# Optimization experiments

Measured on AMD Instinct MI355X. Metric: run time of the kernel, lower is better.

Reference implementation:

```python
import jax, jax.numpy as jnp
import numpy as np

S, R, CM, CZ, C, H = 128, 256, 256, 128, 32, 8
EPS = 1e-5


def layer_norm(x, w, b):
    mu = jnp.mean(x, axis=-1, keepdims=True)
    var = jnp.mean(jnp.square(x - mu), axis=-1, keepdims=True)
    return (x - mu) * jax.lax.rsqrt(var + EPS) * w + b


def setup_inputs() -> dict:
    key = jax.random.key(0)
    ks = jax.random.split(key, 10)
    s = 0.02
    return {
        "m": jax.random.normal(ks[0], (S, R, CM), jnp.float32),
        "z": jax.random.normal(ks[1], (R, R, CZ), jnp.float32),
        "ln_m_w": jnp.ones((CM,), jnp.float32),
        "ln_m_b": jnp.zeros((CM,), jnp.float32),
        "ln_z_w": jnp.ones((CZ,), jnp.float32),
        "ln_z_b": jnp.zeros((CZ,), jnp.float32),
        "Wz": jax.random.normal(ks[2], (CZ, H), jnp.float32) * s,
        "Wq": jax.random.normal(ks[3], (CM, H * C), jnp.float32) * s,
        "Wk": jax.random.normal(ks[4], (CM, H * C), jnp.float32) * s,
        "Wv": jax.random.normal(ks[5], (CM, H * C), jnp.float32) * s,
        "Wg": jax.random.normal(ks[6], (CM, H * C), jnp.float32) * s,
        "bg": jnp.ones((H * C,), jnp.float32),
        "Wo": jax.random.normal(ks[7], (H * C, CM), jnp.float32) * s,
        "bo": jnp.zeros((CM,), jnp.float32),
    }


def reference(m, z, ln_m_w, ln_m_b, ln_z_w, ln_z_b, Wz, Wq, Wk, Wv, Wg, bg, Wo, bo):
    mn = layer_norm(m, ln_m_w, ln_m_b)              # [S,R,CM]
    zn = layer_norm(z, ln_z_w, ln_z_b)              # [R,R,CZ]
    bias = jnp.einsum('qkz,zh->hqk', zn, Wz)        # [H,R,R] pair bias
    q = (mn @ Wq).reshape(S, R, H, C) * (C ** -0.5)
    k = (mn @ Wk).reshape(S, R, H, C)
    v = (mn @ Wv).reshape(S, R, H, C)
    logits = jnp.einsum('sqhc,skhc->shqk', q, k) + bias[None]  # [S,H,R,R]
    a = jax.nn.softmax(logits, axis=-1)
    o = jnp.einsum('shqk,skhc->sqhc', a, v)         # [S,R,H,C]
    g = jax.nn.sigmoid(mn @ Wg + bg).reshape(S, R, H, C)
    return (g * o).reshape(S, R, H * C) @ Wo + bo   # [S,R,CM]
```

## Files before the change

kernel.cpp:

```cpp
#include <hip/hip_runtime.h>
#include <math.h>

#define S_DIM 128
#define R_DIM 256
#define CM_DIM 256
#define CZ_DIM 128
#define C_DIM 32
#define H_DIM 8
#define HC_DIM 256
#define LN_EPS 1e-5f
#define ZPAD 132
#define HSZ 1048576
#define BIAS_SCALE 16384.0f
#define BIAS_INV (1.0f / 16384.0f)

typedef _Float16 half8 __attribute__((ext_vector_type(8)));
typedef _Float16 half4 __attribute__((ext_vector_type(4)));
typedef float f32x4 __attribute__((ext_vector_type(4)));
typedef short short4v __attribute__((ext_vector_type(4)));
typedef short short8v __attribute__((ext_vector_type(8)));

__device__ __forceinline__ float wave_sum(float v) {
#pragma unroll
    for (int off = 32; off > 0; off >>= 1) v += __shfl_down(v, off);
    return v;
}

__device__ __forceinline__ void gload16(const _Float16* src, _Float16* dst) {
    __builtin_amdgcn_global_load_lds((const __attribute__((address_space(1))) void*)src,
                                     (__attribute__((address_space(3))) void*)dst, 16, 0, 0);
}

__global__ __launch_bounds__(256) void convert_w_kernel(const float* __restrict__ Wq,
                                                        const float* __restrict__ Wk,
                                                        const float* __restrict__ Wv,
                                                        const float* __restrict__ Wg,
                                                        const float* __restrict__ Wo,
                                                        _Float16* __restrict__ w3) {
    int kb = blockIdx.x;
    int mat = blockIdx.y;
    const float* src = (mat == 0) ? Wq : (mat == 1) ? Wk : (mat == 2) ? Wv : (mat == 3) ? Wg : Wo;
    int n = threadIdx.x;
    _Float16 tmp[32];
#pragma unroll
    for (int kk = 0; kk < 32; kk++)
        tmp[kk] = (_Float16)src[(size_t)(kb * 32 + kk) * 256 + n];
    half8* dst = (half8*)(w3 + (size_t)mat * 65536 + (size_t)kb * 8192 + (size_t)n * 32);
#pragma unroll
    for (int i = 0; i < 4; i++) dst[i] = *(half8*)&tmp[i * 8];
}

__global__ __launch_bounds__(64) void prep_wz_kernel(const float* __restrict__ w,
                                                     const float* __restrict__ b,
                                                     const float* __restrict__ Wz,
                                                     float* __restrict__ u_g,
                                                     float* __restrict__ UB) {
    int lane = threadIdx.x;
    float w0 = w[lane], w1 = w[lane + 64];
    float b0 = b[lane], b1 = b[lane + 64];
#pragma unroll
    for (int h = 0; h < H_DIM; h++) {
        float wz0 = Wz[lane * H_DIM + h], wz1 = Wz[(lane + 64) * H_DIM + h];
        float u0 = w0 * wz0, u1 = w1 * wz1;
        u_g[h * ZPAD + lane] = u0;
        u_g[h * ZPAD + lane + 64] = u1;
        float U = wave_sum(u0 + u1);
        float B = wave_sum(b0 * wz0 + b1 * wz1);
        if (lane == 0) { UB[h] = U; UB[8 + h] = B; }
    }
}

__global__ __launch_bounds__(64) void ln_m_kernel(const float* __restrict__ m,
                                                  const float* __restrict__ w,
                                                  const float* __restrict__ b,
                                                  _Float16* __restrict__ mn) {
    int row = blockIdx.x;
    int t = threadIdx.x;
    const float4* mrow = (const float4*)(m + (size_t)row * CM_DIM);
    float4 x = mrow[t];
    float s = x.x + x.y + x.z + x.w;
    float ss = x.x * x.x + x.y * x.y + x.z * x.z + x.w * x.w;
    s = wave_sum(s);
    ss = wave_sum(ss);
    s = __shfl(s, 0);
    ss = __shfl(ss, 0);
    float mean = s * (1.0f / CM_DIM);
    float var = ss * (1.0f / CM_DIM) - mean * mean;
    float rsig = rsqrtf(var + LN_EPS);
    float4 wv = ((const float4*)w)[t];
    float4 bv = ((const float4*)b)[t];
    half4 o;
    o[0] = (_Float16)((x.x - mean) * rsig * wv.x + bv.x);
    o[1] = (_Float16)((x.y - mean) * rsig * wv.y + bv.y);
    o[2] = (_Float16)((x.z - mean) * rsig * wv.z + bv.z);
    o[3] = (_Float16)((x.w - mean) * rsig * wv.w + bv.w);
    *(half4*)(mn + (size_t)row * CM_DIM + t * 4) = o;
}

__global__ __launch_bounds__(256) void ln_z_bias_kernel(const float* __restrict__ z,
                                                        const float* __restrict__ u_g,
                                                        const float* __restrict__ UB,
                                                        short* __restrict__ bias_i) {
    __shared__ __align__(16) float zt[64 * ZPAD];
    __shared__ __align__(16) float ut[8 * ZPAD];
    __shared__ float UBs[16];
    int tid = threadIdx.x;
    int row0 = blockIdx.x * 64;
    for (int i = tid; i < 8 * ZPAD; i += 256) ut[i] = u_g[i];
    if (tid < 16) UBs[tid] = UB[tid];
    const float4* zsrc = (const float4*)(z + (size_t)row0 * CZ_DIM);
#pragma unroll
    for (int i = 0; i < 8; i++) {
        int idx = tid + i * 256;
        float4 v = zsrc[idx];
        int r = idx >> 5, c4 = (idx & 31) * 4;
        *(float4*)&zt[r * ZPAD + c4] = v;
    }
    __syncthreads();
    int r = tid >> 2, p = tid & 3;
    const float* zr = &zt[r * ZPAD];
    const float* u0p = &ut[p * ZPAD];
    const float* u1p = &ut[(p + 4) * ZPAD];
    float s = 0.f, ss = 0.f, a0 = 0.f, a1 = 0.f;
#pragma unroll
    for (int c = 0; c < CZ_DIM; c += 4) {
        float4 x = *(const float4*)&zr[c];
        float4 uu0 = *(const float4*)&u0p[c];
        float4 uu1 = *(const float4*)&u1p[c];
        s += x.x + x.y + x.z + x.w;
        ss += x.x * x.x + x.y * x.y + x.z * x.z + x.w * x.w;
        a0 += x.x * uu0.x + x.y * uu0.y + x.z * uu0.z + x.w * uu0.w;
        a1 += x.x * uu1.x + x.y * uu1.y + x.z * uu1.z + x.w * uu1.w;
    }
    float mu = s * (1.0f / CZ_DIM);
    float var = ss * (1.0f / CZ_DIM) - mu * mu;
    float rsig = rsqrtf(var + LN_EPS);
    int row = row0 + r;
    float b0v = rsig * (a0 - mu * UBs[p]) + UBs[8 + p];
    float b1v = rsig * (a1 - mu * UBs[4 + p]) + UBs[12 + p];
    int i0 = (int)rintf(b0v * BIAS_SCALE);
    int i1 = (int)rintf(b1v * BIAS_SCALE);
    i0 = i0 > 32767 ? 32767 : (i0 < -32768 ? -32768 : i0);
    i1 = i1 > 32767 ? 32767 : (i1 < -32768 ? -32768 : i1);
    bias_i[(size_t)p * 65536 + row] = (short)i0;
    bias_i[(size_t)(p + 4) * 65536 + row] = (short)i1;
}

__global__ __launch_bounds__(256, 3) void proj_mfma_kernel(const _Float16* __restrict__ A,
                                                           const _Float16* __restrict__ w3,
                                                           const float* __restrict__ bg,
                                                           _Float16* __restrict__ qh,
                                                           _Float16* __restrict__ kh,
                                                           _Float16* __restrict__ vh,
                                                           _Float16* __restrict__ gh) {
    __shared__ _Float16 Bs[2][64 * 128];
    __shared__ _Float16 Os[64 * 132];
    int m0 = blockIdx.x * 64;
    int col0 = blockIdx.y * 128;
    int tid = threadIdx.x, lane = tid & 63, wave = tid >> 6;
    int lrow = lane & 15, g = lane >> 4;
    int wr = wave >> 1, wc = wave & 1;
    const float qscale = 0.17677669529663687f;

    half8 afr[2][8];
#pragma unroll
    for (int mf = 0; mf < 2; mf++)
#pragma unroll
        for (int kb = 0; kb < 8; kb++)
            afr[mf][kb] = *(const half8*)(A + (size_t)(m0 + wr * 32 + mf * 16 + lrow) * 256 +
                                          kb * 32 + g * 8);

#define STAGE_B(T, BUF)                                                              \
    {                                                                                \
        int mat_ = (T) >> 2, kp_ = (T) & 3;                                          \
        _Float16* dst_ = &Bs[BUF][0];                                                \
        const _Float16* src_ = w3 + (size_t)mat_ * 65536 + (size_t)kp_ * 16384;      \
        _Pragma("unroll") for (int i_ = 0; i_ < 4; i_++) {                           \
            int j_ = tid + i_ * 256;                                                 \
            int n_ = j_ >> 3, cL_ = j_ & 7;                                          \
            int c_ = cL_ ^ (n_ & 7);                                                 \
            int kbL_ = c_ >> 2, q_ = c_ & 3;                                         \
            gload16(src_ + (size_t)kbL_ * 8192 + (size_t)(col0 + n_) * 32 + q_ * 8,  \
                    dst_ + (size_t)j_ * 8);                                          \
        }                                                                            \
    }

    STAGE_B(0, 0);
    STAGE_B(1, 1);
    __syncthreads();

    f32x4 acc[2][4];
    for (int t = 0; t < 16; t++) {
        int buf = t & 1;
        int mat = t >> 2, kp = t & 3;
        if (kp == 0) {
#pragma unroll
            for (int i = 0; i < 2; i++)
#pragma unroll
                for (int j = 0; j < 4; j++) acc[i][j] = (f32x4){0.f, 0.f, 0.f, 0.f};
        }
#pragma unroll
        for (int kbL = 0; kbL < 2; kbL++) {
            int kb = kp * 2 + kbL;
            half8 bf[4];
#pragma unroll
            for (int nf = 0; nf < 4; nf++) {
                int col = wc * 64 + nf * 16 + lrow;
                int chunk = (kbL * 4 + g) ^ (col & 7);
                bf[nf] = *(half8*)&Bs[buf][(size_t)(col * 8 + chunk) * 8];
            }
#pragma unroll
            for (int mf = 0; mf < 2; mf++)
#pragma unroll
                for (int nf = 0; nf < 4; nf++)
                    acc[mf][nf] = __builtin_amdgcn_mfma_f32_16x16x32_f16(afr[mf][kb], bf[nf],
                                                                         acc[mf][nf], 0, 0, 0);
        }
        if (kp == 3) {
#pragma unroll
            for (int mf = 0; mf < 2; mf++)
#pragma unroll
                for (int nf = 0; nf < 4; nf++)
#pragma unroll
                    for (int ri = 0; ri < 4; ri++) {
                        int srow = wr * 32 + mf * 16 + g * 4 + ri;
                        int scol = wc * 64 + nf * 16 + lrow;
                        float v = acc[mf][nf][ri];
                        if (mat == 0) v *= qscale;
                        if (mat == 3) v = 1.0f / (1.0f + __expf(-(v + bg[col0 + scol])));
                        Os[srow * 132 + scol] = (_Float16)v;
                    }
            __syncthreads();
            if (mat < 3) {
                _Float16* Out = (mat == 0) ? qh : (mat == 1) ? kh : vh;
#pragma unroll
                for (int j = 0; j < 4; j++) {
                    int hh = (col0 >> 5) + j;
                    int row = tid >> 2, cOff = (tid & 3) * 8;
                    half8 v8 = *(half8*)&Os[row * 132 + j * 32 + cOff];
                    *(half8*)(Out + (size_t)hh * HSZ + (size_t)(m0 + row) * 32 + cOff) = v8;
                }
            } else {
#pragma unroll
                for (int i = 0; i < 4; i++) {
                    int c2 = tid + i * 256;
                    int row = c2 >> 4, cOff = (c2 & 15) * 8;
                    half8 v8 = *(half8*)&Os[row * 132 + cOff];
                    *(half8*)(gh + (size_t)(m0 + row) * 256 + col0 + cOff) = v8;
                }
            }
        }
        __syncthreads();
        if (t + 2 < 16) STAGE_B(t + 2, buf);
    }
#undef STAGE_B
}

__global__ __launch_bounds__(512, 1) void attn_mfma_kernel(const _Float16* __restrict__ qh,
                                                           const _Float16* __restrict__ kh,
                                                           const _Float16* __restrict__ vh,
                                                           const _Float16* __restrict__ gh,
                                                           const short* __restrict__ bias_i,
                                                           _Float16* __restrict__ oh) {
    __shared__ short bias_s[256][264];
    __shared__ _Float16 K_s[64][40];
    __shared__ _Float16 VT_s[32][72];
    int h = blockIdx.x, sg = blockIdx.y;
    int tid = threadIdx.x;
    int lane = tid & 63, wave = tid >> 6;
    int lrow = lane & 15, g = lane >> 4, lk8 = g * 8;
    int qw = wave * 32;

    const short* bsrc = bias_i + (size_t)h * 65536;
#pragma unroll
    for (int i = 0; i < 16; i++) {
        int e = (tid + i * 512) * 8;
        short8v v = *(const short8v*)(bsrc + e);
        *(short8v*)&bias_s[e >> 8][e & 255] = v;
    }

    const _Float16* qbase = qh + (size_t)h * HSZ;
    const _Float16* kbase = kh + (size_t)h * HSZ;
    const _Float16* vbase = vh + (size_t)h * HSZ;
    _Float16* obase = oh + (size_t)h * HSZ;

    bool isK = (wave < 4);
    int key = (tid & 255) >> 2, koff = (tid & 3) * 8;
    int vkey = tid & 63, vc0 = ((tid >> 6) & 3) * 8;

    for (int si = 0; si < 4; si++) {
        int s = sg * 4 + si;
        half8 qfr[2];
#pragma unroll
        for (int qf = 0; qf < 2; qf++)
            qfr[qf] = *(const half8*)(qbase + (size_t)(s * 256 + qw + qf * 16 + lrow) * 32 + lk8);

        f32x4 oaccT[2][2];
        float m_run[2], l_run[2];
#pragma unroll
        for (int qf = 0; qf < 2; qf++) {
            oaccT[qf][0] = (f32x4){0.f, 0.f, 0.f, 0.f};
            oaccT[qf][1] = (f32x4){0.f, 0.f, 0.f, 0.f};
            m_run[qf] = -1e30f;
            l_run[qf] = 0.f;
        }

        half8 stg;
        if (isK) stg = *(const half8*)(kbase + (size_t)(s * 256 + key) * 32 + koff);
        else     stg = *(const half8*)(vbase + (size_t)(s * 256 + vkey) * 32 + vc0);

        for (int kb = 0; kb < 4; kb++) {
            __syncthreads();
            if (isK) {
                *(half8*)&K_s[key][koff] = stg;
            } else {
#pragma unroll
                for (int j = 0; j < 8; j++) VT_s[vc0 + j][vkey] = stg[j];
            }
            if (kb < 3) {
                int nk = (kb + 1) * 64;
                if (isK) stg = *(const half8*)(kbase + (size_t)(s * 256 + nk + key) * 32 + koff);
                else     stg = *(const half8*)(vbase + (size_t)(s * 256 + nk + vkey) * 32 + vc0);
            }
            __syncthreads();

            half8 kfr[4];
#pragma unroll
            for (int kf = 0; kf < 4; kf++) kfr[kf] = *(half8*)&K_s[kf * 16 + lrow][lk8];

#pragma unroll
            for (int qf = 0; qf < 2; qf++) {
                f32x4 sf[4];
#pragma unroll
                for (int kf = 0; kf < 4; kf++) {
                    f32x4 zero = (f32x4){0.f, 0.f, 0.f, 0.f};
                    sf[kf] = __builtin_amdgcn_mfma_f32_16x16x32_f16(kfr[kf], qfr[qf], zero, 0, 0, 0);
                }
                int q = qw + qf * 16 + lrow;
#pragma unroll
                for (int kf = 0; kf < 4; kf++) {
                    short4v bh = *(short4v*)&bias_s[q][kb * 64 + kf * 16 + 4 * g];
#pragma unroll
                    for (int ri = 0; ri < 4; ri++) sf[kf][ri] += (float)bh[ri] * BIAS_INV;
                }
                float tm = -1e30f;
#pragma unroll
                for (int kf = 0; kf < 4; kf++)
#pragma unroll
                    for (int ri = 0; ri < 4; ri++) tm = fmaxf(tm, sf[kf][ri]);
                tm = fmaxf(tm, __shfl_xor(tm, 16));
                tm = fmaxf(tm, __shfl_xor(tm, 32));
                float nm = fmaxf(m_run[qf], tm);
                float sc = __expf(m_run[qf] - nm);
                m_run[qf] = nm;
                oaccT[qf][0] *= sc;
                oaccT[qf][1] *= sc;
                float p[4][4];
                float rs = 0.f;
#pragma unroll
                for (int kf = 0; kf < 4; kf++)
#pragma unroll
                    for (int ri = 0; ri < 4; ri++) {
                        float pv = __expf(sf[kf][ri] - nm);
                        p[kf][ri] = pv;
                        rs += pv;
                    }
                rs += __shfl_xor(rs, 16);
                rs += __shfl_xor(rs, 32);
                l_run[qf] = l_run[qf] * sc + rs;
                unsigned w8[8];
#pragma unroll
                for (int kf = 0; kf < 4; kf++)
#pragma unroll
                    for (int t = 0; t < 2; t++) {
                        union { _Float16 hh[2]; unsigned u; } pk;
                        pk.hh[0] = (_Float16)p[kf][2 * t];
                        pk.hh[1] = (_Float16)p[kf][2 * t + 1];
                        w8[2 * kf + t] = pk.u;
                    }
#pragma unroll
                for (int ks = 0; ks < 2; ks++) {
                    union { unsigned u[4]; half8 h8; } pb;
#pragma unroll
                    for (int u = 0; u < 4; u++) {
                        int srcl = ((g & 1) * 2 + (u >> 1)) * 16 + lrow;
                        unsigned lo_sh = (unsigned)__shfl((int)w8[4 * ks + (u & 1)], srcl);
                        unsigned hi_sh = (unsigned)__shfl((int)w8[4 * ks + (u & 1) + 2], srcl);
                        pb.u[u] = (g >> 1) ? hi_sh : lo_sh;
                    }
#pragma unroll
                    for (int cf = 0; cf < 2; cf++) {
                        half8 va = *(half8*)&VT_s[cf * 16 + lrow][ks * 32 + lk8];
                        oaccT[qf][cf] =
                            __builtin_amdgcn_mfma_f32_16x16x32_f16(va, pb.h8, oaccT[qf][cf], 0, 0, 0);
                    }
                }
            }
        }
#pragma unroll
        for (int qf = 0; qf < 2; qf++) {
            float inv = 1.0f / l_run[qf];
            int q = qw + qf * 16 + lrow;
#pragma unroll
            for (int cf = 0; cf < 2; cf++) {
                half4 gv4 = *(const half4*)(gh + (size_t)(s * 256 + q) * 256 + h * 32 + cf * 16 + 4 * g);
                half4 o4;
#pragma unroll
                for (int ri = 0; ri < 4; ri++)
                    o4[ri] = (_Float16)(oaccT[qf][cf][ri] * inv * (float)gv4[ri]);
                *(half4*)(obase + (size_t)(s * 256 + q) * 32 + cf * 16 + 4 * g) = o4;
            }
        }
    }
}

__global__ __launch_bounds__(256, 4) void out_mfma_kernel(const _Float16* __restrict__ oh,
                                                          const _Float16* __restrict__ w3o,
                                                          const float* __restrict__ bo,
                                                          float* __restrict__ out) {
    __shared__ _Float16 Bs[2][64 * 128];
    int m0 = blockIdx.x * 64;
    int col0 = blockIdx.y * 128;
    int tid = threadIdx.x, lane = tid & 63, wave = tid >> 6;
    int lrow = lane & 15, g = lane >> 4;
    int wr = wave >> 1, wc = wave & 1;

    half8 afr[2][8];
#pragma unroll
    for (int mf = 0; mf < 2; mf++)
#pragma unroll
        for (int kb = 0; kb < 8; kb++)
            afr[mf][kb] = *(const half8*)(oh + (size_t)kb * HSZ +
                                          (size_t)(m0 + wr * 32 + mf * 16 + lrow) * 32 + g * 8);

#define STAGE_BO(T, BUF)                                                             \
    {                                                                                \
        int kp_ = (T);                                                               \
        _Float16* dst_ = &Bs[BUF][0];                                                \
        const _Float16* src_ = w3o + (size_t)kp_ * 16384;                            \
        _Pragma("unroll") for (int i_ = 0; i_ < 4; i_++) {                           \
            int j_ = tid + i_ * 256;                                                 \
            int n_ = j_ >> 3, cL_ = j_ & 7;                                          \
            int c_ = cL_ ^ (n_ & 7);                                                 \
            int kbL_ = c_ >> 2, q_ = c_ & 3;                                         \
            gload16(src_ + (size_t)kbL_ * 8192 + (size_t)(col0 + n_) * 32 + q_ * 8,  \
                    dst_ + (size_t)j_ * 8);                                          \
        }                                                                            \
    }

    STAGE_BO(0, 0);
    STAGE_BO(1, 1);
    __syncthreads();

    f32x4 acc[2][4];
#pragma unroll
    for (int i = 0; i < 2; i++)
#pragma unroll
        for (int j = 0; j < 4; j++) acc[i][j] = (f32x4){0.f, 0.f, 0.f, 0.f};

    for (int t = 0; t < 4; t++) {
        int buf = t & 1;
#pragma unroll
        for (int kbL = 0; kbL < 2; kbL++) {
            int kb = t * 2 + kbL;
            half8 bf[4];
#pragma unroll
            for (int nf = 0; nf < 4; nf++) {
                int col = wc * 64 + nf * 16 + lrow;
                int chunk = (kbL * 4 + g) ^ (col & 7);
                bf[nf] = *(half8*)&Bs[buf][(size_t)(col * 8 + chunk) * 8];
            }
#pragma unroll
            for (int mf = 0; mf < 2; mf++)
#pragma unroll
                for (int nf = 0; nf < 4; nf++)
                    acc[mf][nf] = __builtin_amdgcn_mfma_f32_16x16x32_f16(afr[mf][kb], bf[nf],
                                                                         acc[mf][nf], 0, 0, 0);
        }
        __syncthreads();
        if (t + 2 < 4) STAGE_BO(t + 2, buf);
    }
#undef STAGE_BO

#pragma unroll
    for (int mf = 0; mf < 2; mf++)
#pragma unroll
        for (int nf = 0; nf < 4; nf++)
#pragma unroll
            for (int ri = 0; ri < 4; ri++) {
                int row = m0 + wr * 32 + mf * 16 + g * 4 + ri;
                int col = col0 + wc * 64 + nf * 16 + lrow;
                out[(size_t)row * 256 + col] = acc[mf][nf][ri] + bo[col];
            }
}

extern "C" void kernel_launch(void* const* d_in, const int* in_sizes, int n_in,
                              void* d_out, int out_size, void* d_ws, size_t ws_size,
                              hipStream_t stream) {
    const float* m = (const float*)d_in[0];
    const float* z = (const float*)d_in[1];
    const float* ln_m_w = (const float*)d_in[2];
    const float* ln_m_b = (const float*)d_in[3];
    const float* ln_z_w = (const float*)d_in[4];
    const float* ln_z_b = (const float*)d_in[5];
    const float* Wz = (const float*)d_in[6];
    const float* Wq = (const float*)d_in[7];
    const float* Wk = (const float*)d_in[8];
    const float* Wv = (const float*)d_in[9];
    const float* Wg = (const float*)d_in[10];
    const float* bg = (const float*)d_in[11];
    const float* Wo = (const float*)d_in[12];
    const float* bo = (const float*)d_in[13];
    float* out = (float*)d_out;

    const size_t NE = (size_t)S_DIM * R_DIM * CM_DIM;
    _Float16* hb = (_Float16*)d_ws;
    _Float16* mn_h = hb;
    _Float16* qh = hb + NE;
    _Float16* kh = hb + 2 * NE;
    _Float16* vh = hb + 3 * NE;
    _Float16* gh = hb + 4 * NE;
    _Float16* oh = hb + 5 * NE;
    _Float16* w3 = hb + 6 * NE;
    float* u_g = (float*)(hb + 6 * NE + 5 * 65536);
    float* UB = u_g + 8 * ZPAD;
    short* bias_i = (short*)(UB + 16);

    hipLaunchKernelGGL(convert_w_kernel, dim3(8, 5), dim3(256), 0, stream,
                       Wq, Wk, Wv, Wg, Wo, w3);
    hipLaunchKernelGGL(prep_wz_kernel, dim3(1), dim3(64), 0, stream,
                       ln_z_w, ln_z_b, Wz, u_g, UB);
    hipLaunchKernelGGL(ln_m_kernel, dim3(S_DIM * R_DIM), dim3(64), 0, stream,
                       m, ln_m_w, ln_m_b, mn_h);
    hipLaunchKernelGGL(ln_z_bias_kernel, dim3(1024), dim3(256), 0, stream,
                       z, u_g, UB, bias_i);
    hipLaunchKernelGGL(proj_mfma_kernel, dim3(512, 2), dim3(256), 0, stream,
                       mn_h, w3, bg, qh, kh, vh, gh);
    hipLaunchKernelGGL(attn_mfma_kernel, dim3(H_DIM, 32), dim3(512), 0, stream,
                       qh, kh, vh, gh, bias_i, oh);
    hipLaunchKernelGGL(out_mfma_kernel, dim3(512, 2), dim3(256), 0, stream,
                       oh, w3 + 4 * 65536, bo, out);
}
```

Baseline: 126.3 us.

## Restructure attention kernel: one block per (head, sequence), full K/V in LDS, bias from global

```diff
diff --git a/kernel.cpp b/kernel.cpp
--- a/kernel.cpp
+++ b/kernel.cpp
@@ -256,160 +256,132 @@
 #undef STAGE_B
 }
 
-__global__ __launch_bounds__(512, 1) void attn_mfma_kernel(const _Float16* __restrict__ qh,
+__global__ __launch_bounds__(256, 4) void attn_mfma_kernel(const _Float16* __restrict__ qh,
                                                            const _Float16* __restrict__ kh,
                                                            const _Float16* __restrict__ vh,
                                                            const _Float16* __restrict__ gh,
                                                            const short* __restrict__ bias_i,
                                                            _Float16* __restrict__ oh) {
-    __shared__ short bias_s[256][264];
-    __shared__ _Float16 K_s[64][40];
-    __shared__ _Float16 VT_s[32][72];
-    int h = blockIdx.x, sg = blockIdx.y;
-    int tid = threadIdx.x;
-    int lane = tid & 63, wave = tid >> 6;
+    __shared__ _Float16 K_s[256][40];
+    __shared__ _Float16 VT_s[32][264];
+    int h = blockIdx.x, s = blockIdx.y;
+    int tid = threadIdx.x, lane = tid & 63, wave = tid >> 6;
     int lrow = lane & 15, g = lane >> 4, lk8 = g * 8;
-    int qw = wave * 32;
-
-    const short* bsrc = bias_i + (size_t)h * 65536;
-#pragma unroll
-    for (int i = 0; i < 16; i++) {
-        int e = (tid + i * 512) * 8;
-        short8v v = *(const short8v*)(bsrc + e);
-        *(short8v*)&bias_s[e >> 8][e & 255] = v;
-    }
-
+    int qw = wave * 64;
     const _Float16* qbase = qh + (size_t)h * HSZ;
     const _Float16* kbase = kh + (size_t)h * HSZ;
     const _Float16* vbase = vh + (size_t)h * HSZ;
     _Float16* obase = oh + (size_t)h * HSZ;
-
-    bool isK = (wave < 4);
-    int key = (tid & 255) >> 2, koff = (tid & 3) * 8;
-    int vkey = tid & 63, vc0 = ((tid >> 6) & 3) * 8;
-
-    for (int si = 0; si < 4; si++) {
-        int s = sg * 4 + si;
-        half8 qfr[2];
-#pragma unroll
-        for (int qf = 0; qf < 2; qf++)
-            qfr[qf] = *(const half8*)(qbase + (size_t)(s * 256 + qw + qf * 16 + lrow) * 32 + lk8);
-
-        f32x4 oaccT[2][2];
-        float m_run[2], l_run[2];
-#pragma unroll
-        for (int qf = 0; qf < 2; qf++) {
-            oaccT[qf][0] = (f32x4){0.f, 0.f, 0.f, 0.f};
-            oaccT[qf][1] = (f32x4){0.f, 0.f, 0.f, 0.f};
-            m_run[qf] = -1e30f;
-            l_run[qf] = 0.f;
-        }
-
-        half8 stg;
-        if (isK) stg = *(const half8*)(kbase + (size_t)(s * 256 + key) * 32 + koff);
-        else     stg = *(const half8*)(vbase + (size_t)(s * 256 + vkey) * 32 + vc0);
-
-        for (int kb = 0; kb < 4; kb++) {
-            __syncthreads();
-            if (isK) {
-                *(half8*)&K_s[key][koff] = stg;
-            } else {
-#pragma unroll
-                for (int j = 0; j < 8; j++) VT_s[vc0 + j][vkey] = stg[j];
+    const short* brow = bias_i + (size_t)h * 65536;
+
+#pragma unroll
+    for (int i = 0; i < 4; i++) {
+        int idx = i * 256 + tid;
+        int key = idx >> 2, c0 = (idx & 3) * 8;
+        half8 kv = *(const half8*)(kbase + (size_t)(s * 256 + key) * 32 + c0);
+        *(half8*)&K_s[key][c0] = kv;
+        half8 vv = *(const half8*)(vbase + (size_t)(s * 256 + key) * 32 + c0);
+#pragma unroll
+        for (int j = 0; j < 8; j++) VT_s[c0 + j][key] = vv[j];
+    }
+    half8 qfr[4];
+#pragma unroll
+    for (int qf = 0; qf < 4; qf++)
+        qfr[qf] = *(const half8*)(qbase + (size_t)(s * 256 + qw + qf * 16 + lrow) * 32 + lk8);
+    __syncthreads();
+
+    f32x4 oaccT[4][2];
+    float m_run[4], l_run[4];
+#pragma unroll
+    for (int qf = 0; qf < 4; qf++) {
+        oaccT[qf][0] = (f32x4){0.f, 0.f, 0.f, 0.f};
+        oaccT[qf][1] = (f32x4){0.f, 0.f, 0.f, 0.f};
+        m_run[qf] = -1e30f;
+        l_run[qf] = 0.f;
+    }
+
+    for (int kb = 0; kb < 4; kb++) {
+        half8 kfr[4];
+#pragma unroll
+        for (int kf = 0; kf < 4; kf++) kfr[kf] = *(half8*)&K_s[kb * 64 + kf * 16 + lrow][lk8];
+
+#pragma unroll
+        for (int qf = 0; qf < 4; qf++) {
+            int q = qw + qf * 16 + lrow;
+            short4v bh[4];
+#pragma unroll
+            for (int kf = 0; kf < 4; kf++)
+                bh[kf] = *(const short4v*)(brow + (size_t)q * 256 + kb * 64 + kf * 16 + 4 * g);
+            f32x4 sf[4];
+#pragma unroll
+            for (int kf = 0; kf < 4; kf++) {
+                f32x4 zero = (f32x4){0.f, 0.f, 0.f, 0.f};
+                sf[kf] = __builtin_amdgcn_mfma_f32_16x16x32_f16(kfr[kf], qfr[qf], zero, 0, 0, 0);
             }
-            if (kb < 3) {
-                int nk = (kb + 1) * 64;
-                if (isK) stg = *(const half8*)(kbase + (size_t)(s * 256 + nk + key) * 32 + koff);
-                else     stg = *(const half8*)(vbase + (size_t)(s * 256 + nk + vkey) * 32 + vc0);
-            }
-            __syncthreads();
-
-            half8 kfr[4];
-#pragma unroll
-            for (int kf = 0; kf < 4; kf++) kfr[kf] = *(half8*)&K_s[kf * 16 + lrow][lk8];
-
-#pragma unroll
-            for (int qf = 0; qf < 2; qf++) {
-                f32x4 sf[4];
-#pragma unroll
-                for (int kf = 0; kf < 4; kf++) {
-                    f32x4 zero = (f32x4){0.f, 0.f, 0.f, 0.f};
-                    sf[kf] = __builtin_amdgcn_mfma_f32_16x16x32_f16(kfr[kf], qfr[qf], zero, 0, 0, 0);
+#pragma unroll
+            for (int kf = 0; kf < 4; kf++)
+#pragma unroll
+                for (int ri = 0; ri < 4; ri++) sf[kf][ri] += (float)bh[kf][ri] * BIAS_INV;
+            float tm = -1e30f;
+#pragma unroll
+            for (int kf = 0; kf < 4; kf++)
+#pragma unroll
+                for (int ri = 0; ri < 4; ri++) tm = fmaxf(tm, sf[kf][ri]);
+            tm = fmaxf(tm, __shfl_xor(tm, 16));
+            tm = fmaxf(tm, __shfl_xor(tm, 32));
+            float nm = fmaxf(m_run[qf], tm);
+            float sc = __expf(m_run[qf] - nm);
+            m_run[qf] = nm;
+            oaccT[qf][0] *= sc;
+            oaccT[qf][1] *= sc;
+            float rs = 0.f;
+            unsigned w8[8];
+#pragma unroll
+            for (int kf = 0; kf < 4; kf++)
+#pragma unroll
+                for (int t = 0; t < 2; t++) {
+                    float pv0 = __expf(sf[kf][2 * t] - nm);
+                    float pv1 = __expf(sf[kf][2 * t + 1] - nm);
+                    rs += pv0 + pv1;
+                    union { _Float16 hh[2]; unsigned u; } pk;
+                    pk.hh[0] = (_Float16)pv0;
+                    pk.hh[1] = (_Float16)pv1;
+                    w8[2 * kf + t] = pk.u;
                 }
-                int q = qw + qf * 16 + lrow;
-#pragma unroll
-                for (int kf = 0; kf < 4; kf++) {
-                    short4v bh = *(short4v*)&bias_s[q][kb * 64 + kf * 16 + 4 * g];
-#pragma unroll
-                    for (int ri = 0; ri < 4; ri++) sf[kf][ri] += (float)bh[ri] * BIAS_INV;
+            rs += __shfl_xor(rs, 16);
+            rs += __shfl_xor(rs, 32);
+            l_run[qf] = l_run[qf] * sc + rs;
+#pragma unroll
+            for (int ks = 0; ks < 2; ks++) {
+                union { unsigned u[4]; half8 h8; } pb;
+#pragma unroll
+                for (int u = 0; u < 4; u++) {
+                    int srcl = ((g & 1) * 2 + (u >> 1)) * 16 + lrow;
+                    unsigned lo_sh = (unsigned)__shfl((int)w8[4 * ks + (u & 1)], srcl);
+                    unsigned hi_sh = (unsigned)__shfl((int)w8[4 * ks + (u & 1) + 2], srcl);
+                    pb.u[u] = (g >> 1) ? hi_sh : lo_sh;
                 }
-                float tm = -1e30f;
-#pragma unroll
-                for (int kf = 0; kf < 4; kf++)
-#pragma unroll
-                    for (int ri = 0; ri < 4; ri++) tm = fmaxf(tm, sf[kf][ri]);
-                tm = fmaxf(tm, __shfl_xor(tm, 16));
-                tm = fmaxf(tm, __shfl_xor(tm, 32));
-                float nm = fmaxf(m_run[qf], tm);
-                float sc = __expf(m_run[qf] - nm);
-                m_run[qf] = nm;
-                oaccT[qf][0] *= sc;
-                oaccT[qf][1] *= sc;
-                float p[4][4];
-                float rs = 0.f;
-#pragma unroll
-                for (int kf = 0; kf < 4; kf++)
-#pragma unroll
-                    for (int ri = 0; ri < 4; ri++) {
-                        float pv = __expf(sf[kf][ri] - nm);
-                        p[kf][ri] = pv;
-                        rs += pv;
-                    }
-                rs += __shfl_xor(rs, 16);
-                rs += __shfl_xor(rs, 32);
-                l_run[qf] = l_run[qf] * sc + rs;
-                unsigned w8[8];
-#pragma unroll
-                for (int kf = 0; kf < 4; kf++)
-#pragma unroll
-                    for (int t = 0; t < 2; t++) {
-                        union { _Float16 hh[2]; unsigned u; } pk;
-                        pk.hh[0] = (_Float16)p[kf][2 * t];
-                        pk.hh[1] = (_Float16)p[kf][2 * t + 1];
-                        w8[2 * kf + t] = pk.u;
-                    }
-#pragma unroll
-                for (int ks = 0; ks < 2; ks++) {
-                    union { unsigned u[4]; half8 h8; } pb;
-#pragma unroll
-                    for (int u = 0; u < 4; u++) {
-                        int srcl = ((g & 1) * 2 + (u >> 1)) * 16 + lrow;
-                        unsigned lo_sh = (unsigned)__shfl((int)w8[4 * ks + (u & 1)], srcl);
-                        unsigned hi_sh = (unsigned)__shfl((int)w8[4 * ks + (u & 1) + 2], srcl);
-                        pb.u[u] = (g >> 1) ? hi_sh : lo_sh;
-                    }
-#pragma unroll
-                    for (int cf = 0; cf < 2; cf++) {
-                        half8 va = *(half8*)&VT_s[cf * 16 + lrow][ks * 32 + lk8];
-                        oaccT[qf][cf] =
-                            __builtin_amdgcn_mfma_f32_16x16x32_f16(va, pb.h8, oaccT[qf][cf], 0, 0, 0);
-                    }
+#pragma unroll
+                for (int cf = 0; cf < 2; cf++) {
+                    half8 va = *(half8*)&VT_s[cf * 16 + lrow][kb * 64 + ks * 32 + lk8];
+                    oaccT[qf][cf] =
+                        __builtin_amdgcn_mfma_f32_16x16x32_f16(va, pb.h8, oaccT[qf][cf], 0, 0, 0);
                 }
             }
         }
-#pragma unroll
-        for (int qf = 0; qf < 2; qf++) {
-            float inv = 1.0f / l_run[qf];
-            int q = qw + qf * 16 + lrow;
-#pragma unroll
-            for (int cf = 0; cf < 2; cf++) {
-                half4 gv4 = *(const half4*)(gh + (size_t)(s * 256 + q) * 256 + h * 32 + cf * 16 + 4 * g);
-                half4 o4;
-#pragma unroll
-                for (int ri = 0; ri < 4; ri++)
-                    o4[ri] = (_Float16)(oaccT[qf][cf][ri] * inv * (float)gv4[ri]);
-                *(half4*)(obase + (size_t)(s * 256 + q) * 32 + cf * 16 + 4 * g) = o4;
-            }
+    }
+#pragma unroll
+    for (int qf = 0; qf < 4; qf++) {
+        float inv = 1.0f / l_run[qf];
+        int q = qw + qf * 16 + lrow;
+#pragma unroll
+        for (int cf = 0; cf < 2; cf++) {
+            half4 gv4 = *(const half4*)(gh + (size_t)(s * 256 + q) * 256 + h * 32 + cf * 16 + 4 * g);
+            half4 o4;
+#pragma unroll
+            for (int ri = 0; ri < 4; ri++)
+                o4[ri] = (_Float16)(oaccT[qf][cf][ri] * inv * (float)gv4[ri]);
+            *(half4*)(obase + (size_t)(s * 256 + q) * 32 + cf * 16 + 4 * g) = o4;
         }
     }
 }
@@ -536,7 +508,7 @@
                        z, u_g, UB, bias_i);
     hipLaunchKernelGGL(proj_mfma_kernel, dim3(512, 2), dim3(256), 0, stream,
                        mn_h, w3, bg, qh, kh, vh, gh);
-    hipLaunchKernelGGL(attn_mfma_kernel, dim3(H_DIM, 32), dim3(512), 0, stream,
+    hipLaunchKernelGGL(attn_mfma_kernel, dim3(H_DIM, S_DIM), dim3(256), 0, stream,
                        qh, kh, vh, gh, bias_i, oh);
     hipLaunchKernelGGL(out_mfma_kernel, dim3(512, 2), dim3(256), 0, stream,
                        oh, w3 + 4 * 65536, bo, out);
```

After: 147.5 us. 1.17x slower.
